# Optimization experiments

Measured on AMD Instinct MI355X. Metric: run time of the kernel, lower is better.

The kernel has to match this reference:

```python
import jax, jax.numpy as jnp
import numpy as np

N, E, E_LBL = 50000, 800000, 200000
D_IN, H = 128, 128


def setup_inputs() -> dict:
    key = jax.random.key(0)
    ks = jax.random.split(key, 12)
    s = 0.05
    return {
        "x": jax.random.normal(ks[0], (N, D_IN), jnp.float32),
        "edge_index": jax.random.randint(ks[1], (2, E), 0, N, jnp.int64),
        "edge_label_index": jax.random.randint(ks[2], (2, E_LBL), 0, N, jnp.int64),
        "pre_w": jax.random.normal(ks[3], (D_IN, H), jnp.float32) * s,
        "pre_b": jax.random.normal(ks[4], (H,), jnp.float32) * s,
        "Wx": jax.random.normal(ks[5], (3, 2, H, H), jnp.float32) * s,  # gates z,r,h x cheb orders T0,T1
        "bx": jax.random.normal(ks[6], (3, H), jnp.float32) * s,
        "Wh": jax.random.normal(ks[7], (3, 2, H, H), jnp.float32) * s,
        "bh": jax.random.normal(ks[8], (3, H), jnp.float32) * s,
        "post_w": jax.random.normal(ks[9], (H, 2), jnp.float32) * s,
        "post_b": jax.random.normal(ks[10], (2,), jnp.float32) * s,
    }


def reference(x, edge_index, edge_label_index, pre_w, pre_b, Wx, bx, Wh, bh, post_w, post_b):
    n = x.shape[0]
    src, dst = edge_index[0], edge_index[1]

    # Scaled Chebyshev Laplacian (sym norm, lambda_max=2): L_hat = -D^{-1/2} A D^{-1/2}
    # (diagonal of L_hat is exactly 0, so only off-diagonal edge terms remain).
    deg = jax.ops.segment_sum(jnp.ones_like(src, dtype=x.dtype), src, num_segments=n)
    dinv = jnp.where(deg > 0, jax.lax.rsqrt(jnp.maximum(deg, 1.0)), 0.0)
    w = -(dinv[src] * dinv[dst])  # [E]

    def lap(v):  # L_hat @ v : gather src rows, weight, scatter-add at dst
        return jax.ops.segment_sum(w[:, None] * v[src], dst, num_segments=n)

    def cheb(v, Lv, W2, b):  # ChebConv K=2: T0(v)@W0 + T1(v)@W1 + b
        return v @ W2[0] + Lv @ W2[1] + b

    # pre: Linear(input_dim -> hidden)
    Xh = x @ pre_w + pre_b  # [N, H]
    LX = lap(Xh)

    # GConvGRU single step, H0 = 0
    Hc = jnp.zeros_like(Xh)
    LH = lap(Hc)
    Z = jax.nn.sigmoid(cheb(Xh, LX, Wx[0], bx[0]) + cheb(Hc, LH, Wh[0], bh[0]))
    R = jax.nn.sigmoid(cheb(Xh, LX, Wx[1], bx[1]) + cheb(Hc, LH, Wh[1], bh[1]))
    HR = Hc * R
    LHR = lap(HR)
    Ht = jnp.tanh(cheb(Xh, LX, Wx[2], bx[2]) + cheb(HR, LHR, Wh[2], bh[2]))
    Hc = Z * Hc + (1.0 - Z) * Ht

    h = jax.nn.relu(Hc)
    # link decoder: gather endpoints, hadamard, Linear(H->2), sum over logits
    hprod = h[edge_label_index[0]] * h[edge_label_index[1]]  # [E_lbl, H]
    out = hprod @ post_w + post_b  # [E_lbl, 2]
    return jnp.sum(out, axis=-1)  # [E_lbl]
```

## Files before the change

### kernel.cpp

```cpp
#include <hip/hip_runtime.h>
#include <math.h>


#define RND 2048
#define SORT_CAP 1536
#define CAPB 6144

typedef __attribute__((ext_vector_type(4))) float f32x4;
typedef __attribute__((ext_vector_type(8))) short short8;
typedef __attribute__((ext_vector_type(4))) unsigned u32x4;
typedef __attribute__((ext_vector_type(4))) int i32x4;

static __device__ __forceinline__ unsigned short f2b(float f) {
  union { float f; unsigned u; } v; v.f = f;
  unsigned r = (v.u + 0x7fffu + ((v.u >> 16) & 1u)) >> 16;
  return (unsigned short)r;
}
static __device__ __forceinline__ float b2f(unsigned short s) {
  union { unsigned u; float f; } v; v.u = ((unsigned)s) << 16;
  return v.f;
}

__global__ __launch_bounds__(256) void prep_kernel(const float* __restrict__ pre_w, const float* __restrict__ Wx,
                                                   const float* __restrict__ bx, const float* __restrict__ bh,
                                                   const float* __restrict__ post_w, const float* __restrict__ post_b,
                                                   unsigned short* __restrict__ Bt1c, unsigned short* __restrict__ Btc2,
                                                   float* __restrict__ fb2, float* __restrict__ pwsum,
                                                   int* __restrict__ binPos) {
  int e = blockIdx.x * 256 + threadIdx.x;
  if (e < 512) binPos[e * 16] = (e & 255) * CAPB;
  if (e < 16384) {
    int kc = e >> 12, r = e & 4095, col = r >> 5, kk = r & 31;
    Bt1c[e] = f2b(pre_w[(kc * 32 + kk) * 128 + col]);
  }
  int e2 = e - 16384;
  if (e2 >= 0 && e2 < 65536) {
    int kc = e2 >> 13, r = e2 & 8191, cB = r >> 5, kk = r & 31;
    int k = kc * 32 + kk, half = k >> 7, ki = k & 127;
    int cb = cB >> 7, r7 = cB & 127, nw6 = r7 >> 6, u2 = r7 & 63;
    int g = (u2 >= 32) ? 2 : 0, hcol = cb * 64 + nw6 * 32 + (u2 & 31);
    Btc2[e2] = f2b(Wx[((g * 2 + half) * 128 + ki) * 128 + hcol]);
  }
  int e3 = e - (16384 + 65536);
  if (e3 >= 0 && e3 < 256) {
    int cB = e3;
    int cb = cB >> 7, r7 = cB & 127, nw6 = r7 >> 6, u2 = r7 & 63;
    int g = (u2 >= 32) ? 2 : 0, hcol = cb * 64 + nw6 * 32 + (u2 & 31);
    fb2[cB] = bx[g * 128 + hcol] + bh[g * 128 + hcol];
  }
  int e4 = e - (16384 + 65536 + 256);
  if (e4 >= 0 && e4 < 128) pwsum[e4] = post_w[2 * e4] + post_w[2 * e4 + 1];
  if (e4 == 128) pwsum[128] = post_b[0] + post_b[1];
}

union SMemU {
  struct { unsigned short As[128 * 40]; unsigned short Bs[128 * 40]; } g;
  struct { unsigned ent[RND]; int hist[256], lstart[256], lofs[256], gbase[256], wsum[4];
           unsigned char ebin[RND], sb[RND]; } s;
};

__global__ __launch_bounds__(256) void mega1_kernel(const float* __restrict__ x,
                                                    const unsigned short* __restrict__ Bt1c,
                                                    const float* __restrict__ pre_b,
                                                    unsigned short* __restrict__ Xq,
                                                    const int* __restrict__ ei, int* __restrict__ binPos,
                                                    unsigned* __restrict__ bins,
                                                    unsigned char* __restrict__ sbins,
                                                    int N, int E, int RB) {
  __shared__ SMemU sm;
  const int t = threadIdx.x;

  if ((int)blockIdx.x < RB) {
    unsigned short* As = sm.g.As;
    unsigned short* Bs = sm.g.Bs;
    const int r0 = blockIdx.x * 128;
    const int w = t >> 6, lane = t & 63;
    const int m = lane & 15, q = lane >> 4;
    const int mw = (w >> 1) * 64, nw = (w & 1) * 64;

    f32x4 acc[4][4];
#pragma unroll
    for (int i = 0; i < 4; ++i)
#pragma unroll
      for (int j = 0; j < 4; ++j) acc[i][j] = {0.f, 0.f, 0.f, 0.f};

    const int arow = t >> 1, aseg = t & 1;
    const bool arow_ok = (r0 + arow) < N;
    const float* asrc0 = &x[(size_t)(r0 + arow) * 128 + aseg * 16];

    float4 cav[4]; short8 cbv0, cbv1;
    {
      if (arow_ok) {
#pragma unroll
        for (int i = 0; i < 4; ++i) cav[i] = *(const float4*)(asrc0 + i * 4);
      } else {
#pragma unroll
        for (int i = 0; i < 4; ++i) cav[i] = make_float4(0.f, 0.f, 0.f, 0.f);
      }
      const char* src = (const char*)Bt1c + t * 32;
      cbv0 = *(const short8*)src;
      cbv1 = *(const short8*)(src + 16);
    }

    for (int kc = 0; kc < 4; ++kc) {
      __syncthreads();
      {
        short8 t0, t1;
#pragma unroll
        for (int i = 0; i < 2; ++i) {
          t0[i * 4 + 0] = (short)f2b(cav[i].x); t0[i * 4 + 1] = (short)f2b(cav[i].y);
          t0[i * 4 + 2] = (short)f2b(cav[i].z); t0[i * 4 + 3] = (short)f2b(cav[i].w);
          t1[i * 4 + 0] = (short)f2b(cav[i + 2].x); t1[i * 4 + 1] = (short)f2b(cav[i + 2].y);
          t1[i * 4 + 2] = (short)f2b(cav[i + 2].z); t1[i * 4 + 3] = (short)f2b(cav[i + 2].w);
        }
        *(short8*)&As[arow * 40 + aseg * 16] = t0;
        *(short8*)&As[arow * 40 + aseg * 16 + 8] = t1;
        int bcol = t >> 1, boff = (t & 1) * 16;
        *(short8*)&Bs[bcol * 40 + boff] = cbv0;
        *(short8*)&Bs[bcol * 40 + boff + 8] = cbv1;
      }
      float4 nav[4]; short8 nbv0, nbv1;
      if (kc < 3) {
        if (arow_ok) {
          const float* src = asrc0 + (kc + 1) * 32;
#pragma unroll
          for (int i = 0; i < 4; ++i) nav[i] = *(const float4*)(src + i * 4);
        } else {
#pragma unroll
          for (int i = 0; i < 4; ++i) nav[i] = make_float4(0.f, 0.f, 0.f, 0.f);
        }
        const char* src = (const char*)Bt1c + (size_t)(kc + 1) * 8192 + t * 32;
        nbv0 = *(const short8*)src;
        nbv1 = *(const short8*)(src + 16);
      }
      __syncthreads();
      short8 af[4], bf[4];
#pragma unroll
      for (int i = 0; i < 4; ++i) af[i] = *(const short8*)&As[(mw + i * 16 + m) * 40 + q * 8];
#pragma unroll
      for (int j = 0; j < 4; ++j) bf[j] = *(const short8*)&Bs[(nw + j * 16 + m) * 40 + q * 8];
#pragma unroll
      for (int i = 0; i < 4; ++i)
#pragma unroll
        for (int j = 0; j < 4; ++j)
          acc[i][j] = __builtin_amdgcn_mfma_f32_16x16x32_bf16(af[i], bf[j], acc[i][j], 0, 0, 0);
      if (kc < 3) {
#pragma unroll
        for (int i = 0; i < 4; ++i) cav[i] = nav[i];
        cbv0 = nbv0; cbv1 = nbv1;
      }
    }

#pragma unroll
    for (int i = 0; i < 4; ++i) {
      int rb2 = r0 + mw + i * 16 + q * 4;
#pragma unroll
      for (int j = 0; j < 4; ++j) {
        int col = nw + j * 16 + m;
        float bias = pre_b[col];
#pragma unroll
        for (int r = 0; r < 4; ++r) {
          int row = rb2 + r;
          if (row < N) Xq[(size_t)row * 128 + col] = f2b(acc[i][j][r] + bias);
        }
      }
    }
    return;
  }

  unsigned* ent = sm.s.ent;
  unsigned char* ebin = sm.s.ebin;
  unsigned char* sb = sm.s.sb;
  int* hist = sm.s.hist;
  int* lstart = sm.s.lstart;
  int* lofs = sm.s.lofs;
  int* gbase = sm.s.gbase;
  int* wsum = sm.s.wsum;
  const int sbid = (int)blockIdx.x - RB;
  const int snum = (int)gridDim.x - RB;
  const int w = t >> 6, lane = t & 63;
  for (long long base = (long long)sbid * RND; base < E; base += (long long)snum * RND) {
    int cnt = (int)(((long long)E - base < RND) ? (E - base) : RND);
    if (t < 256) hist[t] = 0;
    __syncthreads();
    int my_s[8], my_d[8];
    {
      long long e0 = base + (long long)t * 8;
      if (e0 + 8 <= E && 8 * t + 8 <= cnt) {
        const i32x4* ps = (const i32x4*)&ei[e0];
        const i32x4* pd = (const i32x4*)&ei[E + e0];
        i32x4 s0 = ps[0], s1 = ps[1], d0 = pd[0], d1 = pd[1];
#pragma unroll
        for (int u = 0; u < 4; ++u) { my_s[u] = s0[u]; my_d[u] = d0[u]; }
#pragma unroll
        for (int u = 0; u < 4; ++u) { my_s[4 + u] = s1[u]; my_d[4 + u] = d1[u]; }
      } else {
#pragma unroll
        for (int u = 0; u < 8; ++u) {
          int i = t * 8 + u;
          my_s[u] = -1;
          if (i < cnt) { my_s[u] = ei[base + i]; my_d[u] = ei[E + base + i]; }
        }
      }
#pragma unroll
      for (int u = 0; u < 8; ++u)
        if (my_s[u] >= 0) atomicAdd(&hist[my_d[u] >> 8], 1);
    }
    __syncthreads();
    {
      int h = hist[t];
      hist[t] = 0;
      int v = h;
#pragma unroll
      for (int dd = 1; dd < 64; dd <<= 1) { int uu = __shfl_up(v, dd); if (lane >= dd) v += uu; }
      if (lane == 63) wsum[w] = v;
      __syncthreads();
      int woff = 0;
#pragma unroll
      for (int ww = 0; ww < 3; ++ww) if (ww < w) woff += wsum[ww];
      int excl = v - h + woff;
      lstart[t] = excl; lofs[t] = excl;
      if (h > 0) gbase[t] = atomicAdd(&binPos[t * 16], h);
    }
    __syncthreads();
#pragma unroll
    for (int u = 0; u < 8; ++u) {
      if (my_s[u] >= 0) {
        int b = my_d[u] >> 8;
        int p = atomicAdd(&lofs[b], 1);
        ent[p] = (unsigned)my_s[u] | ((unsigned)(my_d[u] & 255) << 16) | ((unsigned)b << 24);
        atomicAdd(&hist[my_s[u] >> 8], 1);
      }
    }
    __syncthreads();
    for (int i = t; i < cnt; i += 256) {
      unsigned e = ent[i];
      int b = e >> 24;
      int pos = gbase[b] + (i - lstart[b]);
      if (pos < (b + 1) * CAPB) bins[pos] = e;
    }
    __syncthreads();
    {
      int h = hist[t];
      int v = h;
#pragma unroll
      for (int dd = 1; dd < 64; dd <<= 1) { int uu = __shfl_up(v, dd); if (lane >= dd) v += uu; }
      if (lane == 63) wsum[w] = v;
      __syncthreads();
      int woff = 0;
#pragma unroll
      for (int ww = 0; ww < 3; ++ww) if (ww < w) woff += wsum[ww];
      int excl = v - h + woff;
      lstart[t] = excl; lofs[t] = excl;
      if (h > 0) gbase[t] = atomicAdd(&binPos[(256 + t) * 16], h);
    }
    __syncthreads();
#pragma unroll
    for (int u = 0; u < 8; ++u) {
      if (my_s[u] >= 0) {
        int b = my_s[u] >> 8;
        int p = atomicAdd(&lofs[b], 1);
        sb[p] = (unsigned char)(my_s[u] & 255);
        ebin[p] = (unsigned char)b;
      }
    }
    __syncthreads();
    for (int i = t; i < cnt; i += 256) {
      int b = ebin[i];
      int pos = gbase[b] + (i - lstart[b]);
      if (pos < (b + 1) * CAPB) sbins[pos] = sb[i];
    }
    __syncthreads();
  }
}

__global__ __launch_bounds__(512) void deghist_kernel(const unsigned char* __restrict__ sbins,
                                                      const int* __restrict__ binPos,
                                                      const unsigned short* __restrict__ Xq,
                                                      unsigned short* __restrict__ Xs,
                                                      float* __restrict__ dinvNeg, int N) {
  __shared__ int h[256];
  __shared__ float sdi[256];
  const int t = threadIdx.x;
  const int bin = blockIdx.x;
  if (t < 256) h[t] = 0;
  __syncthreads();
  int T2 = binPos[(256 + bin) * 16] - bin * CAPB;
  if (T2 > CAPB) T2 = CAPB;
  const unsigned char* __restrict__ p = sbins + (size_t)bin * CAPB;
  for (int i = t; i < T2; i += 512) atomicAdd(&h[p[i]], 1);
  __syncthreads();
  if (t < 256) {
    int node = bin * 256 + t;
    float di = h[t] > 0 ? rsqrtf((float)h[t]) : 0.0f;
    sdi[t] = di;
    if (node < N) dinvNeg[node] = -di;
  }
  __syncthreads();
  const int wv = t >> 6, lane = t & 63;
  const int g4 = lane >> 4, sl = lane & 15;
#pragma unroll
  for (int it = 0; it < 8; ++it) {
    int r = wv * 32 + it * 4 + g4;
    int rnode = bin * 256 + r;
    if (rnode < N) {
      float di_r = sdi[r];
      u32x4 v = *(const u32x4*)((const char*)Xq + (size_t)rnode * 256 + sl * 16);
      u32x4 o;
#pragma unroll
      for (int k = 0; k < 4; ++k) {
        union { unsigned u32; float f; } fl, fh;
        fl.u32 = v[k] << 16; fh.u32 = v[k] & 0xffff0000u;
        o[k] = (unsigned)f2b(fl.f * di_r) | ((unsigned)f2b(fh.f * di_r) << 16);
      }
      *(u32x4*)((char*)Xs + (size_t)rnode * 256 + sl * 16) = o;
    }
  }
}

__global__ __launch_bounds__(512) void lap_bin_kernel(const unsigned short* __restrict__ Xs,
                                                      unsigned short* __restrict__ LXc,
                                                      const unsigned* __restrict__ bins,
                                                      const int* __restrict__ binPos,
                                                      const float* __restrict__ dinvNeg, int N) {
  __shared__ unsigned eLDS[CAPB];
  __shared__ unsigned short sortS[SORT_CAP];
  __shared__ int hist[32], start[32], off[32];
  const int t = threadIdx.x;
  const int bin = blockIdx.x >> 3, qt = blockIdx.x & 7;
  const int lo = bin * CAPB;
  int T = binPos[bin * 16] - lo;
  if (T > CAPB) T = CAPB;
  const unsigned* __restrict__ ebase = &bins[lo];
  if (t < 32) hist[t] = 0;
  __syncthreads();
  for (int i = t; i < T; i += 512) {
    unsigned e = ebase[i];
    eLDS[i] = e;
    int dl = (e >> 16) & 255;
    if ((dl >> 5) == qt) atomicAdd(&hist[dl & 31], 1);
  }
  __syncthreads();
  if (t < 32) {
    int h = hist[t];
    int v = h;
#pragma unroll
    for (int d = 1; d < 32; d <<= 1) {
      int u = __shfl_up(v, d);
      if (t >= d) v += u;
    }
    start[t] = v - h;
    off[t] = v - h;
  }
  __syncthreads();
  for (int i = t; i < T; i += 512) {
    unsigned e = eLDS[i];
    int dl = (e >> 16) & 255;
    if ((dl >> 5) == qt) {
      int p = atomicAdd(&off[dl & 31], 1);
      if (p < SORT_CAP) sortS[p] = (unsigned short)(e & 0xFFFFu);
    }
  }
  __syncthreads();
  const int wv = t >> 6, lane = t & 63;
  const int g4 = lane >> 4, sl = lane & 15;
  for (int n = wv; n < 32; n += 8) {
    int node = bin * 256 + qt * 32 + n;
    if (node >= N) break;
    int st = start[n], cnum = hist[n];
    float acc[8] = {0.f, 0.f, 0.f, 0.f, 0.f, 0.f, 0.f, 0.f};
    for (int j = 0; j < cnum; j += 8) {
#pragma unroll
      for (int u = 0; u < 2; ++u) {
        int idx = j + u * 4 + g4;
        bool val = idx < cnum;
        int s = sortS[st + (val ? idx : 0)];
        u32x4 vv = *(const u32x4*)((const char*)Xs + (size_t)s * 256 + sl * 16);
        if (val) {
#pragma unroll
          for (int k = 0; k < 4; ++k) {
            union { unsigned u32; float f; } fl, fh;
            fl.u32 = vv[k] << 16; fh.u32 = vv[k] & 0xffff0000u;
            acc[2 * k] += fl.f;
            acc[2 * k + 1] += fh.f;
          }
        }
      }
    }
#pragma unroll
    for (int k = 0; k < 8; ++k) {
      acc[k] += __shfl_xor(acc[k], 16);
      acc[k] += __shfl_xor(acc[k], 32);
    }
    if (g4 == 0) {
      float wd = dinvNeg[node];
      u32x4 o;
#pragma unroll
      for (int k = 0; k < 4; ++k)
        o[k] = (unsigned)f2b(acc[2 * k] * wd) | ((unsigned)f2b(acc[2 * k + 1] * wd) << 16);
      *(u32x4*)((char*)LXc + (size_t)node * 256 + sl * 16) = o;
    }
  }
}

__global__ __launch_bounds__(256) void gemm2_mfma(const unsigned short* __restrict__ Xq,
                                                  const unsigned short* __restrict__ LXc,
                                                  const unsigned short* __restrict__ Btc2,
                                                  const float* __restrict__ fb2,
                                                  unsigned short* __restrict__ hb, int N) {
  __shared__ unsigned short As[128 * 40];
  __shared__ unsigned short Bs[128 * 40];
  const int t = threadIdx.x;
  const int rb = blockIdx.x >> 1, cb = blockIdx.x & 1;
  const int r0 = rb * 128;
  const int w = t >> 6, lane = t & 63;
  const int m = lane & 15, q = lane >> 4;
  const int mw = (w >> 1) * 64, nw = (w & 1) * 64;

  f32x4 acc[4][4];
#pragma unroll
  for (int i = 0; i < 4; ++i)
#pragma unroll
    for (int j = 0; j < 4; ++j) acc[i][j] = {0.f, 0.f, 0.f, 0.f};

  const int arow = t >> 1;
  const int aoff = (t & 1) * 32;
  const char* aXq = (const char*)Xq + (size_t)(r0 + arow) * 256 + aoff;
  const char* aLX = (const char*)LXc + (size_t)(r0 + arow) * 256 + aoff;
  const char* bsrc0 = (const char*)Btc2 + (size_t)cb * 8192 + t * 32;

  short8 cav0, cav1, cbv0, cbv1;
  cav0 = *(const short8*)aXq;
  cav1 = *(const short8*)(aXq + 16);
  cbv0 = *(const short8*)bsrc0;
  cbv1 = *(const short8*)(bsrc0 + 16);

  for (int kc = 0; kc < 8; ++kc) {
    __syncthreads();
    *(short8*)&As[arow * 40 + (aoff >> 1)] = cav0;
    *(short8*)&As[arow * 40 + (aoff >> 1) + 8] = cav1;
    {
      int bcol = t >> 1, boff = (t & 1) * 16;
      *(short8*)&Bs[bcol * 40 + boff] = cbv0;
      *(short8*)&Bs[bcol * 40 + boff + 8] = cbv1;
    }
    short8 nav0, nav1, nbv0, nbv1;
    if (kc < 7) {
      int kn = kc + 1;
      const char* asrc = (kn < 4) ? (aXq + kn * 64) : (aLX + (kn - 4) * 64);
      nav0 = *(const short8*)asrc;
      nav1 = *(const short8*)(asrc + 16);
      const char* bsrc = bsrc0 + (size_t)kn * 16384;
      nbv0 = *(const short8*)bsrc;
      nbv1 = *(const short8*)(bsrc + 16);
    }
    __syncthreads();
    short8 af[4], bf[4];
#pragma unroll
    for (int i = 0; i < 4; ++i) af[i] = *(const short8*)&As[(mw + i * 16 + m) * 40 + q * 8];
#pragma unroll
    for (int j = 0; j < 4; ++j) bf[j] = *(const short8*)&Bs[(nw + j * 16 + m) * 40 + q * 8];
#pragma unroll
    for (int i = 0; i < 4; ++i)
#pragma unroll
      for (int j = 0; j < 4; ++j)
        acc[i][j] = __builtin_amdgcn_mfma_f32_16x16x32_bf16(af[i], bf[j], acc[i][j], 0, 0, 0);
    if (kc < 7) { cav0 = nav0; cav1 = nav1; cbv0 = nbv0; cbv1 = nbv1; }
  }

#pragma unroll
  for (int i = 0; i < 4; ++i) {
    int rbase = r0 + mw + i * 16 + q * 4;
#pragma unroll
    for (int jz = 0; jz < 2; ++jz) {
      int cBz = cb * 128 + nw + jz * 16 + m;
      int hc = cb * 64 + (nw >> 1) + jz * 16 + m;
      float bz = fb2[cBz], bt = fb2[cBz + 32];
#pragma unroll
      for (int r = 0; r < 4; ++r) {
        int row = rbase + r;
        if (row < N) {
          float zp = acc[i][jz][r] + bz;
          float tp = acc[i][jz + 2][r] + bt;
          float zs = 1.0f / (1.0f + __expf(-zp));
          float th = tanhf(tp);
          hb[(size_t)row * 128 + hc] = f2b(fmaxf((1.0f - zs) * th, 0.0f));
        }
      }
    }
  }
}

__global__ __launch_bounds__(256) void decoder_kernel(const unsigned short* __restrict__ hb,
                                                      const int* __restrict__ eli,
                                                      const float* __restrict__ pwsum, float* __restrict__ out, int M) {
  int t = threadIdx.x;
  int i = blockIdx.x * 16 + (t >> 4);
  int l = t & 15;
  if (i >= M) return;
  int a = eli[i], b = eli[M + i];
  int k = l * 8;
  short8 va = *(const short8*)&hb[(size_t)a * 128 + k];
  short8 vb = *(const short8*)&hb[(size_t)b * 128 + k];
  const float4* pwp = (const float4*)&pwsum[k];
  float4 p0 = pwp[0], p1 = pwp[1];
  float s = 0.0f;
  s += b2f((unsigned short)va[0]) * b2f((unsigned short)vb[0]) * p0.x;
  s += b2f((unsigned short)va[1]) * b2f((unsigned short)vb[1]) * p0.y;
  s += b2f((unsigned short)va[2]) * b2f((unsigned short)vb[2]) * p0.z;
  s += b2f((unsigned short)va[3]) * b2f((unsigned short)vb[3]) * p0.w;
  s += b2f((unsigned short)va[4]) * b2f((unsigned short)vb[4]) * p1.x;
  s += b2f((unsigned short)va[5]) * b2f((unsigned short)vb[5]) * p1.y;
  s += b2f((unsigned short)va[6]) * b2f((unsigned short)vb[6]) * p1.z;
  s += b2f((unsigned short)va[7]) * b2f((unsigned short)vb[7]) * p1.w;
#pragma unroll
  for (int off = 8; off; off >>= 1) s += __shfl_xor(s, off);
  if (l == 0) out[i] = s + pwsum[128];
}

extern "C" void kernel_launch(void* const* d_in, const int* in_sizes, int n_in,
                              void* d_out, int out_size, void* d_ws, size_t ws_size,
                              hipStream_t stream) {
  const float* x      = (const float*)d_in[0];
  const int*   ei     = (const int*)d_in[1];
  const int*   eli    = (const int*)d_in[2];
  const float* pre_w  = (const float*)d_in[3];
  const float* pre_b  = (const float*)d_in[4];
  const float* Wx     = (const float*)d_in[5];
  const float* bx     = (const float*)d_in[6];
  const float* bh     = (const float*)d_in[8];
  const float* post_w = (const float*)d_in[9];
  const float* post_b = (const float*)d_in[10];
  float* out = (float*)d_out;

  const int N = in_sizes[0] / 128;
  const int E = in_sizes[1] / 2;
  const int M = in_sizes[2] / 2;
  const int RB = (N + 127) / 128;
  const int NBIN = (N + 255) / 256;
  const int SCAT = (E + RND - 1) / RND;

  char* W = (char*)d_ws;
  size_t o = 0;
  float* dinvNeg = (float*)(W + o); o += (size_t)N * 4;
  o = (o + 255) & ~(size_t)255;
  int* binPos = (int*)(W + o);    o += 512 * 16 * 4;
  o = (o + 255) & ~(size_t)255;
  unsigned* bins = (unsigned*)(W + o); o += (size_t)NBIN * CAPB * 4;
  o = (o + 255) & ~(size_t)255;
  unsigned char* sbins = (unsigned char*)(W + o); o += (size_t)NBIN * CAPB;
  o = (o + 255) & ~(size_t)255;
  unsigned short* Xq = (unsigned short*)(W + o);  o += (size_t)RB * 128 * 256;
  unsigned short* Xs = (unsigned short*)(W + o);  o += (size_t)RB * 128 * 256;
  unsigned short* LXc = (unsigned short*)(W + o); o += (size_t)RB * 128 * 256;
  unsigned short* hb = (unsigned short*)(W + o);  o += (size_t)N * 256;
  unsigned short* Bt1c = (unsigned short*)(W + o); o += 32768;
  unsigned short* Btc2 = (unsigned short*)(W + o); o += 131072;
  float* fb2 = (float*)(W + o);  o += 1024;
  float* pwsum = (float*)(W + o); o += 768;

  prep_kernel<<<322, 256, 0, stream>>>(pre_w, Wx, bx, bh, post_w, post_b, Bt1c, Btc2, fb2, pwsum,
                                       binPos);
  mega1_kernel<<<RB + SCAT, 256, 0, stream>>>(x, Bt1c, pre_b, Xq, ei, binPos, bins, sbins, N, E, RB);
  deghist_kernel<<<NBIN, 512, 0, stream>>>(sbins, binPos, Xq, Xs, dinvNeg, N);
  lap_bin_kernel<<<NBIN * 8, 512, 0, stream>>>(Xs, LXc, bins, binPos, dinvNeg, N);
  gemm2_mfma<<<RB * 2, 256, 0, stream>>>(Xq, LXc, Btc2, fb2, hb, N);
  decoder_kernel<<<(M + 15) / 16, 256, 0, stream>>>(hb, eli, pwsum, out, M);
}
```

Before: 200.9 us.

## Apply source degree weights in Laplacian gather instead of pre-scaled feature copy

The degree kernel now writes only dinv and no longer builds a dinv-scaled bf16 copy of Xq. This removes a full read and write pass over the node features. The Laplacian kernel instead looks up dinv[src] once per edge during its local sort, stores it in shared memory and multiplies it in during accumulation. Each Laplacian block now covers 64 destination nodes instead of 32, halving the block count and the repeated reads of each bin's edge list, at the cost of more shared memory and fewer blocks in flight.

```diff
diff --git a/kernel.cpp b/kernel.cpp
--- a/kernel.cpp
+++ b/kernel.cpp
@@ -274,78 +274,52 @@
   }
 }
 
-__global__ __launch_bounds__(512) void deghist_kernel(const unsigned char* __restrict__ sbins,
+__global__ __launch_bounds__(256) void deghist_kernel(const unsigned char* __restrict__ sbins,
                                                       const int* __restrict__ binPos,
-                                                      const unsigned short* __restrict__ Xq,
-                                                      unsigned short* __restrict__ Xs,
-                                                      float* __restrict__ dinvNeg, int N) {
+                                                      float* __restrict__ dinv, int N) {
   __shared__ int h[256];
-  __shared__ float sdi[256];
   const int t = threadIdx.x;
   const int bin = blockIdx.x;
-  if (t < 256) h[t] = 0;
+  h[t] = 0;
   __syncthreads();
   int T2 = binPos[(256 + bin) * 16] - bin * CAPB;
   if (T2 > CAPB) T2 = CAPB;
   const unsigned char* __restrict__ p = sbins + (size_t)bin * CAPB;
-  for (int i = t; i < T2; i += 512) atomicAdd(&h[p[i]], 1);
+  for (int i = t; i < T2; i += 256) atomicAdd(&h[p[i]], 1);
   __syncthreads();
-  if (t < 256) {
-    int node = bin * 256 + t;
-    float di = h[t] > 0 ? rsqrtf((float)h[t]) : 0.0f;
-    sdi[t] = di;
-    if (node < N) dinvNeg[node] = -di;
-  }
-  __syncthreads();
-  const int wv = t >> 6, lane = t & 63;
-  const int g4 = lane >> 4, sl = lane & 15;
-#pragma unroll
-  for (int it = 0; it < 8; ++it) {
-    int r = wv * 32 + it * 4 + g4;
-    int rnode = bin * 256 + r;
-    if (rnode < N) {
-      float di_r = sdi[r];
-      u32x4 v = *(const u32x4*)((const char*)Xq + (size_t)rnode * 256 + sl * 16);
-      u32x4 o;
-#pragma unroll
-      for (int k = 0; k < 4; ++k) {
-        union { unsigned u32; float f; } fl, fh;
-        fl.u32 = v[k] << 16; fh.u32 = v[k] & 0xffff0000u;
-        o[k] = (unsigned)f2b(fl.f * di_r) | ((unsigned)f2b(fh.f * di_r) << 16);
-      }
-      *(u32x4*)((char*)Xs + (size_t)rnode * 256 + sl * 16) = o;
-    }
-  }
-}
-
-__global__ __launch_bounds__(512) void lap_bin_kernel(const unsigned short* __restrict__ Xs,
+  int node = bin * 256 + t;
+  if (node < N) dinv[node] = h[t] > 0 ? rsqrtf((float)h[t]) : 0.0f;
+}
+
+__global__ __launch_bounds__(512) void lap_bin_kernel(const unsigned short* __restrict__ Xq,
                                                       unsigned short* __restrict__ LXc,
                                                       const unsigned* __restrict__ bins,
                                                       const int* __restrict__ binPos,
-                                                      const float* __restrict__ dinvNeg, int N) {
+                                                      const float* __restrict__ dinv, int N) {
   __shared__ unsigned eLDS[CAPB];
   __shared__ unsigned short sortS[SORT_CAP];
-  __shared__ int hist[32], start[32], off[32];
+  __shared__ float sortW[SORT_CAP];
+  __shared__ int hist[64], start[64], off[64];
   const int t = threadIdx.x;
-  const int bin = blockIdx.x >> 3, qt = blockIdx.x & 7;
+  const int bin = blockIdx.x >> 2, qt = blockIdx.x & 3;
   const int lo = bin * CAPB;
   int T = binPos[bin * 16] - lo;
   if (T > CAPB) T = CAPB;
   const unsigned* __restrict__ ebase = &bins[lo];
-  if (t < 32) hist[t] = 0;
+  if (t < 64) hist[t] = 0;
   __syncthreads();
   for (int i = t; i < T; i += 512) {
     unsigned e = ebase[i];
     eLDS[i] = e;
     int dl = (e >> 16) & 255;
-    if ((dl >> 5) == qt) atomicAdd(&hist[dl & 31], 1);
+    if ((dl >> 6) == qt) atomicAdd(&hist[dl & 63], 1);
   }
   __syncthreads();
-  if (t < 32) {
+  if (t < 64) {
     int h = hist[t];
     int v = h;
 #pragma unroll
-    for (int d = 1; d < 32; d <<= 1) {
+    for (int d = 1; d < 64; d <<= 1) {
       int u = __shfl_up(v, d);
       if (t >= d) v += u;
     }
@@ -356,16 +330,20 @@
   for (int i = t; i < T; i += 512) {
     unsigned e = eLDS[i];
     int dl = (e >> 16) & 255;
-    if ((dl >> 5) == qt) {
-      int p = atomicAdd(&off[dl & 31], 1);
-      if (p < SORT_CAP) sortS[p] = (unsigned short)(e & 0xFFFFu);
+    if ((dl >> 6) == qt) {
+      int p = atomicAdd(&off[dl & 63], 1);
+      if (p < SORT_CAP) {
+        int s = (int)(e & 0xFFFFu);
+        sortS[p] = (unsigned short)s;
+        sortW[p] = dinv[s];
+      }
     }
   }
   __syncthreads();
   const int wv = t >> 6, lane = t & 63;
   const int g4 = lane >> 4, sl = lane & 15;
-  for (int n = wv; n < 32; n += 8) {
-    int node = bin * 256 + qt * 32 + n;
+  for (int n = wv; n < 64; n += 8) {
+    int node = bin * 256 + qt * 64 + n;
     if (node >= N) break;
     int st = start[n], cnum = hist[n];
     float acc[8] = {0.f, 0.f, 0.f, 0.f, 0.f, 0.f, 0.f, 0.f};
@@ -374,15 +352,17 @@
       for (int u = 0; u < 2; ++u) {
         int idx = j + u * 4 + g4;
         bool val = idx < cnum;
-        int s = sortS[st + (val ? idx : 0)];
-        u32x4 vv = *(const u32x4*)((const char*)Xs + (size_t)s * 256 + sl * 16);
+        int si = st + (val ? idx : 0);
+        int s = sortS[si];
+        float ws = sortW[si];
+        u32x4 vv = *(const u32x4*)((const char*)Xq + (size_t)s * 256 + sl * 16);
         if (val) {
 #pragma unroll
           for (int k = 0; k < 4; ++k) {
             union { unsigned u32; float f; } fl, fh;
             fl.u32 = vv[k] << 16; fh.u32 = vv[k] & 0xffff0000u;
-            acc[2 * k] += fl.f;
-            acc[2 * k + 1] += fh.f;
+            acc[2 * k] += ws * fl.f;
+            acc[2 * k + 1] += ws * fh.f;
           }
         }
       }
@@ -393,7 +373,7 @@
       acc[k] += __shfl_xor(acc[k], 32);
     }
     if (g4 == 0) {
-      float wd = dinvNeg[node];
+      float wd = -dinv[node];
       u32x4 o;
 #pragma unroll
       for (int k = 0; k < 4; ++k)
@@ -542,7 +522,7 @@
 
   char* W = (char*)d_ws;
   size_t o = 0;
-  float* dinvNeg = (float*)(W + o); o += (size_t)N * 4;
+  float* dinv = (float*)(W + o); o += (size_t)N * 4;
   o = (o + 255) & ~(size_t)255;
   int* binPos = (int*)(W + o);    o += 512 * 16 * 4;
   o = (o + 255) & ~(size_t)255;
@@ -551,7 +531,6 @@
   unsigned char* sbins = (unsigned char*)(W + o); o += (size_t)NBIN * CAPB;
   o = (o + 255) & ~(size_t)255;
   unsigned short* Xq = (unsigned short*)(W + o);  o += (size_t)RB * 128 * 256;
-  unsigned short* Xs = (unsigned short*)(W + o);  o += (size_t)RB * 128 * 256;
   unsigned short* LXc = (unsigned short*)(W + o); o += (size_t)RB * 128 * 256;
   unsigned short* hb = (unsigned short*)(W + o);  o += (size_t)N * 256;
   unsigned short* Bt1c = (unsigned short*)(W + o); o += 32768;
@@ -562,8 +541,8 @@
   prep_kernel<<<322, 256, 0, stream>>>(pre_w, Wx, bx, bh, post_w, post_b, Bt1c, Btc2, fb2, pwsum,
                                        binPos);
   mega1_kernel<<<RB + SCAT, 256, 0, stream>>>(x, Bt1c, pre_b, Xq, ei, binPos, bins, sbins, N, E, RB);
-  deghist_kernel<<<NBIN, 512, 0, stream>>>(sbins, binPos, Xq, Xs, dinvNeg, N);
-  lap_bin_kernel<<<NBIN * 8, 512, 0, stream>>>(Xs, LXc, bins, binPos, dinvNeg, N);
+  deghist_kernel<<<NBIN, 256, 0, stream>>>(sbins, binPos, dinv, N);
+  lap_bin_kernel<<<NBIN * 4, 512, 0, stream>>>(Xq, LXc, bins, binPos, dinv, N);
   gemm2_mfma<<<RB * 2, 256, 0, stream>>>(Xq, LXc, Btc2, fb2, hb, N);
   decoder_kernel<<<(M + 15) / 16, 256, 0, stream>>>(hb, eli, pwsum, out, M);
 }
```

Result: no change. 197.4 us (-1.8%).
